# Kernel optimization log

Hardware: AMD Instinct MI355X
Metric: run time of the kernel (lower is better)

## Reference

```python
import jax, jax.numpy as jnp
import numpy as np

B, L, D, E, K, P = 1024, 320, 128, 8, 2, 96
NOISE_EPS = 0.01
LOSS_COEF = 0.01


def setup_inputs() -> dict:
    key = jax.random.key(0)
    ks = jax.random.split(key, 8)
    return {
        "x": jax.random.normal(ks[0], (B, L, D), jnp.float32),
        "x_mark_enc": jax.random.normal(ks[1], (B, L, 4), jnp.float32),
        "noise": jax.random.normal(ks[2], (B, E), jnp.float32),  # randn_like in torch
        "start_w": jax.random.normal(ks[3], (D, 1), jnp.float32) * 0.05,
        "start_b": jnp.zeros((1,), jnp.float32),
        "w_gate": jax.random.normal(ks[4], (L, E), jnp.float32) * 0.02,
        "w_noise": jax.random.normal(ks[5], (L, E), jnp.float32) * 0.02,
        "expert_w": jax.random.normal(ks[6], (E, L, P), jnp.float32) * (1.0 / np.sqrt(L)),
        "expert_b": jnp.zeros((E, P, D), jnp.float32),
    }


def _norm_cdf(v):
    return 0.5 * (1.0 + jax.lax.erf(v * (1.0 / np.sqrt(2.0)).astype(v.dtype) if hasattr((1.0 / np.sqrt(2.0)), 'astype') else v / jnp.sqrt(jnp.asarray(2.0, v.dtype))))


def _cdf(v):
    # standard normal CDF, Normal(0,1).cdf
    return 0.5 * (1.0 + jax.lax.erf(v / jnp.sqrt(jnp.asarray(2.0, v.dtype))))


def _cv_squared(v):
    eps = 1e-10
    return jnp.var(v, ddof=1) / (jnp.mean(v) ** 2 + eps)


def reference(x, x_mark_enc, noise, start_w, start_b, w_gate, w_noise, expert_b, expert_w):
    # --- noisy top-k gating (train mode) ---
    g = jnp.squeeze(x @ start_w, -1) + start_b  # [B, L]
    clean_logits = g @ w_gate                    # [B, E]
    noise_std = jax.nn.softplus(g @ w_noise) + NOISE_EPS
    noisy_logits = clean_logits + noise * noise_std

    top_logits, top_idx = jax.lax.top_k(noisy_logits, K + 1)  # [B, K+1]
    top_k_gates = jax.nn.softmax(top_logits[:, :K], axis=1)
    gates = jnp.zeros_like(noisy_logits).at[
        jnp.arange(noisy_logits.shape[0])[:, None], top_idx[:, :K]
    ].set(top_k_gates)  # [B, E] sparse gates (zeros elsewhere)

    # --- differentiable load via prob-in-top-k ---
    thr_in = top_logits[:, K:K + 1]       # (k+1)-th noisy value
    thr_out = top_logits[:, K - 1:K]      # k-th noisy value
    clean_c = jnp.where(jnp.isnan(clean_logits), 0.0, clean_logits)
    prob = jnp.where(
        noisy_logits > thr_in,
        _cdf((clean_c - thr_in) / noise_std),
        _cdf((clean_c - thr_out) / noise_std),
    )
    load = prob.sum(0)          # [E]
    importance = gates.sum(0)   # [E]
    balance_loss = LOSS_COEF * (_cv_squared(importance) + _cv_squared(load))

    # --- dispatch/combine: dense-equivalent of SparseDispatcher ---
    # expert e: out_e = einsum('bld,lp->bpd', x, W_e); combine weights = gates
    per_expert = jnp.einsum('bld,elp->ebpd', x, expert_w)          # [E, B, P, D]
    out = jnp.einsum('be,ebpd->bpd', gates, per_expert)
    out = out + jnp.einsum('be,epd->bpd', gates, expert_b)
    regu_sum = jnp.asarray(0.0, jnp.float32)
    return out, balance_loss, regu_sum
```

## Files before the change

kernel.cpp:

```cpp
#include <hip/hip_runtime.h>
#include <hip/hip_bf16.h>

#define Bn 1024
#define Lr 320
#define Dd 128
#define Ee 8
#define Pp 96

typedef short bf16x8 __attribute__((ext_vector_type(8)));
typedef float f32x4 __attribute__((ext_vector_type(4)));
typedef unsigned u32x4 __attribute__((ext_vector_type(4)));
typedef unsigned short u16;

__device__ __forceinline__ float cdf_f(float v) {
    return 0.5f * (1.0f + erff(v * 0.70710678118654752f));
}
__device__ __forceinline__ float softplus_f(float x) {
    return fmaxf(x, 0.0f) + log1pf(expf(-fabsf(x)));
}
__device__ __forceinline__ u16 f2bf(float f) {
    unsigned int u = __float_as_uint(f);
    return (u16)((u + 0x7fffu + ((u >> 16) & 1u)) >> 16);
}
__device__ __forceinline__ float bf2f(u16 u) {
    return __uint_as_float(((unsigned int)u) << 16);
}

__device__ __forceinline__ void gload16(const void* g, void* l) {
    __builtin_amdgcn_global_load_lds(
        (const __attribute__((address_space(1))) void*)g,
        (__attribute__((address_space(3))) void*)l, 16, 0, 0);
}

__global__ __launch_bounds__(256, 8) void g2_kernel(
    const float* __restrict__ x, const float* __restrict__ start_w,
    const float* __restrict__ start_b, const float* __restrict__ w_gate,
    const float* __restrict__ w_noise, float* __restrict__ zbuf)
{
    __shared__ float sred[16];
    const int t  = threadIdx.x;
    const int lc = blockIdx.x;
    const int b  = blockIdx.y;
    const float sb = start_b[0];
    const int f8 = t & 7;

    if (t < 16) sred[t] = 0.f;
    __syncthreads();

    float4 sw[4];
    #pragma unroll
    for (int j = 0; j < 4; ++j) sw[j] = ((const float4*)start_w)[f8 + 8 * j];

    const float* xb = x + ((size_t)b * Lr + lc * 64) * Dd;
    float zc = 0.f, zn = 0.f;
    #pragma unroll
    for (int p2 = 0; p2 < 2; ++p2) {
        const int r = p2 * 32 + (t >> 3);
        float acc = 0.f;
        #pragma unroll
        for (int j = 0; j < 4; ++j) {
            const float4 v = ((const float4*)(xb + (size_t)r * Dd))[f8 + 8 * j];
            acc += v.x * sw[j].x + v.y * sw[j].y + v.z * sw[j].z + v.w * sw[j].w;
        }
        #pragma unroll
        for (int off = 1; off <= 4; off <<= 1) acc += __shfl_xor(acc, off);
        const float gv = acc + sb;
        const int l = lc * 64 + r;
        zc += gv * w_gate[l * Ee + f8];
        zn += gv * w_noise[l * Ee + f8];
    }
    #pragma unroll
    for (int off = 8; off <= 32; off <<= 1) {
        zc += __shfl_xor(zc, off);
        zn += __shfl_xor(zn, off);
    }
    if ((t & 63) < 8) {
        atomicAdd(&sred[f8], zc);
        atomicAdd(&sred[8 + f8], zn);
    }
    __syncthreads();
    if (t < 16) zbuf[(b * 5 + lc) * 16 + t] = sred[t];
}

__global__ __launch_bounds__(256) void tk_tr_kernel(
    const float* __restrict__ zbuf, const float* __restrict__ noise,
    const float* __restrict__ ew, u16* __restrict__ wt,
    float* __restrict__ lossbuf, float* __restrict__ gates_out)
{
    __shared__ float tile[Pp * 33];
    const int t = threadIdx.x;

    if (blockIdx.x >= 4) {
        const int bx = blockIdx.x - 4;
        const int e  = bx / 10;
        const int l0 = (bx - 10 * e) * 32;
        #pragma unroll
        for (int i = 0; i < 12; ++i) {
            const int idx = t + 256 * i;
            const int lp = idx / 96, p = idx - 96 * lp;
            tile[p * 33 + lp] = ew[((size_t)e * Lr + l0 + lp) * Pp + p];
        }
        __syncthreads();
        #pragma unroll
        for (int i = 0; i < 6; ++i) {
            const int g = t + 256 * i;
            const int p = g >> 4, l2 = (g & 15) * 2;
            const unsigned pk = (unsigned)f2bf(tile[p * 33 + l2]) |
                                ((unsigned)f2bf(tile[p * 33 + l2 + 1]) << 16);
            *(unsigned*)&wt[((size_t)(e * Pp + p)) * Lr + l0 + l2] = pk;
        }
        return;
    }

    float* sred = tile;
    const int b = blockIdx.x * 256 + t;

    if (t < 16) sred[t] = 0.f;
    __syncthreads();

    float zc[8], zn[8], nsy[8], sdv[8];
    #pragma unroll
    for (int e = 0; e < 8; ++e) { zc[e] = 0.f; zn[e] = 0.f; }
    #pragma unroll
    for (int lc = 0; lc < 5; ++lc) {
        #pragma unroll
        for (int e = 0; e < 8; ++e) {
            zc[e] += zbuf[(b * 5 + lc) * 16 + e];
            zn[e] += zbuf[(b * 5 + lc) * 16 + 8 + e];
        }
    }
    #pragma unroll
    for (int e = 0; e < 8; ++e) {
        sdv[e] = softplus_f(zn[e]) + 0.01f;
        nsy[e] = zc[e] + noise[b * Ee + e] * sdv[e];
    }

    int i0 = -1, i1 = -1;
    float v0 = -INFINITY, v1 = -INFINITY, v2 = -INFINITY;
    #pragma unroll
    for (int i = 0; i < 8; ++i) if (nsy[i] > v0) { v0 = nsy[i]; i0 = i; }
    #pragma unroll
    for (int i = 0; i < 8; ++i) if (i != i0 && nsy[i] > v1) { v1 = nsy[i]; i1 = i; }
    #pragma unroll
    for (int i = 0; i < 8; ++i) if (i != i0 && i != i1 && nsy[i] > v2) { v2 = nsy[i]; }

    const float ex1 = expf(v1 - v0);
    const float den = 1.f + ex1;
    const float g0 = 1.f / den, g1 = ex1 / den;

    float im[8], pr[8];
    #pragma unroll
    for (int e = 0; e < 8; ++e) {
        im[e] = (e == i0) ? g0 : ((e == i1) ? g1 : 0.f);
        float c = zc[e];
        if (isnan(c)) c = 0.f;
        pr[e] = (nsy[e] > v2) ? cdf_f((c - v2) / sdv[e])
                              : cdf_f((c - v1) / sdv[e]);
        gates_out[b * Ee + e] = im[e];
    }

    #pragma unroll
    for (int off = 1; off <= 32; off <<= 1) {
        #pragma unroll
        for (int e = 0; e < 8; ++e) {
            pr[e] += __shfl_xor(pr[e], off);
            im[e] += __shfl_xor(im[e], off);
        }
    }
    if ((t & 63) == 0) {
        #pragma unroll
        for (int e = 0; e < 8; ++e) {
            atomicAdd(&sred[e], pr[e]);
            atomicAdd(&sred[8 + e], im[e]);
        }
    }
    __syncthreads();
    if (t < 16) lossbuf[blockIdx.x * 16 + t] = sred[t];
}

__global__ __launch_bounds__(512, 2) void mm_kernel(
    const float* __restrict__ x, const u16* __restrict__ wt,
    const float* __restrict__ expert_b, const float* __restrict__ gates,
    const float* __restrict__ lossbuf, float* __restrict__ out)
{
    __shared__ __align__(16) unsigned Ws[2][192 * 16];

    const int tid = threadIdx.x;

    if (blockIdx.x == 0 && tid == 0) {
        float lo[8], im[8];
        #pragma unroll
        for (int i = 0; i < 8; ++i) {
            lo[i] = lossbuf[i]      + lossbuf[16 + i] +
                    lossbuf[32 + i] + lossbuf[48 + i];
            im[i] = lossbuf[8 + i]  + lossbuf[24 + i] +
                    lossbuf[40 + i] + lossbuf[56 + i];
        }
        float ml = 0.f, mi = 0.f;
        #pragma unroll
        for (int i = 0; i < 8; ++i) { ml += lo[i]; mi += im[i]; }
        ml *= 0.125f; mi *= 0.125f;
        float sl = 0.f, si = 0.f;
        #pragma unroll
        for (int i = 0; i < 8; ++i) {
            const float dl = lo[i] - ml, di = im[i] - mi;
            sl += dl * dl; si += di * di;
        }
        const float cvl = (sl / 7.f) / (ml * ml + 1e-10f);
        const float cvi = (si / 7.f) / (mi * mi + 1e-10f);
        float* os = out + (size_t)Bn * Pp * Dd;
        os[0] = 0.01f * (cvi + cvl);
        os[1] = 0.0f;
    }

    const int b    = blockIdx.x;
    const int lane = tid & 63;
    const int wv   = tid >> 6;
    const int hh   = wv >> 2;
    const int nt   = wv & 3;
    const int quad = lane >> 4;
    const int r16  = lane & 15;

    int e0 = 0, e1 = 0; float g0 = 0.f, g1 = 0.f; int cnt = 0;
    #pragma unroll
    for (int e = 0; e < Ee; ++e) {
        const float gv = gates[b * Ee + e];
        if (gv != 0.f) {
            if (cnt == 0) { e0 = e; g0 = gv; }
            else if (cnt == 1) { e1 = e; g1 = gv; }
            ++cnt;
        }
    }

    const u16* w0r = wt + (size_t)e0 * Pp * Lr;
    const u16* w1r = wt + (size_t)e1 * Pp * Lr;

    const int d = hh * 64 + nt * 16 + r16;
    const float* xg = x + ((size_t)b * Lr + 8 * quad) * Dd + d;

    const int wrow = lane >> 2;
    const int wq   = lane & 3;

    auto STAGE_W = [&](int buf, int l0) {
        {
            const int c  = wv;
            const int r  = 16 * c + wrow;
            const int dw = (4 * wq) ^ ((r & 3) << 2);
            const u16* src = (c < 6) ? (w0r + (size_t)r * Lr)
                                     : (w1r + (size_t)(r - 96) * Lr);
            gload16(src + l0 + 2 * dw, (void*)&Ws[buf][c * 256]);
        }
        if (wv < 4) {
            const int c  = 8 + wv;
            const int r  = 16 * c + wrow;
            const int dw = (4 * wq) ^ ((r & 3) << 2);
            const u16* src = w1r + (size_t)(r - 96) * Lr;
            gload16(src + l0 + 2 * dw, (void*)&Ws[buf][c * 256]);
        }
    };

    float xa[8], xb8[8];
    auto LOADX = [&](float* dst, int l0) {
        #pragma unroll
        for (int k = 0; k < 8; ++k)
            dst[k] = xg[(size_t)(l0 + k) * Dd];
    };

    f32x4 a0[6], a1[6];
    #pragma unroll
    for (int m = 0; m < 6; ++m) {
        a0[m] = (f32x4){0.f, 0.f, 0.f, 0.f};
        a1[m] = (f32x4){0.f, 0.f, 0.f, 0.f};
    }

    const int wdw = (4 * quad) ^ ((r16 & 3) << 2);

    union UF { u32x4 q; bf16x8 v; unsigned u[4]; };

    auto COMPUTE = [&](int buf, const float* xv) {
        UF xf;
        #pragma unroll
        for (int k2 = 0; k2 < 4; ++k2)
            xf.u[k2] = (unsigned)f2bf(xv[2 * k2]) |
                       ((unsigned)f2bf(xv[2 * k2 + 1]) << 16);
        #pragma unroll
        for (int m = 0; m < 6; ++m) {
            UF f0, f1;
            f0.q = *(const u32x4*)&Ws[buf][(16 * m + r16) * 16 + wdw];
            f1.q = *(const u32x4*)&Ws[buf][(96 + 16 * m + r16) * 16 + wdw];
            a0[m] = __builtin_amdgcn_mfma_f32_16x16x32_bf16(f0.v, xf.v, a0[m], 0, 0, 0);
            a1[m] = __builtin_amdgcn_mfma_f32_16x16x32_bf16(f1.v, xf.v, a1[m], 0, 0, 0);
        }
    };

    STAGE_W(0, 0);
    LOADX(xa, 0);
    __syncthreads();

    #pragma unroll
    for (int t = 0; t < 10; t += 2) {
        STAGE_W(1, 32 * (t + 1));
        LOADX(xb8, 32 * (t + 1));
        COMPUTE(0, xa);
        __syncthreads();
        if (t + 2 < 10) {
            STAGE_W(0, 32 * (t + 2));
            LOADX(xa, 32 * (t + 2));
        }
        COMPUTE(1, xb8);
        __syncthreads();
    }

    const float* eb0 = expert_b + (size_t)e0 * Pp * Dd;
    const float* eb1 = expert_b + (size_t)e1 * Pp * Dd;
    #pragma unroll
    for (int m = 0; m < 6; ++m) {
        #pragma unroll
        for (int r = 0; r < 4; ++r) {
            const int p = 16 * m + 4 * quad + r;
            out[((size_t)b * Pp + p) * Dd + d] =
                g0 * (a0[m][r] + eb0[p * Dd + d]) +
                g1 * (a1[m][r] + eb1[p * Dd + d]);
        }
    }
}

extern "C" void kernel_launch(void* const* d_in, const int* in_sizes, int n_in,
                              void* d_out, int out_size, void* d_ws, size_t ws_size,
                              hipStream_t stream)
{
    const float* x        = (const float*)d_in[0];
    const float* noise    = (const float*)d_in[2];
    const float* start_w  = (const float*)d_in[3];
    const float* start_b  = (const float*)d_in[4];
    const float* w_gate   = (const float*)d_in[5];
    const float* w_noise  = (const float*)d_in[6];
    const float* expert_w = (const float*)d_in[7];
    const float* expert_b = (const float*)d_in[8];
    float* out            = (float*)d_out;

    float* gates   = (float*)d_ws;
    float* zbuf    = gates + Bn * Ee;
    float* lossbuf = zbuf + Bn * 80;
    u16*   wt      = (u16*)(lossbuf + 64);

    hipLaunchKernelGGL(g2_kernel, dim3(5, Bn), dim3(256), 0, stream,
                       x, start_w, start_b, w_gate, w_noise, zbuf);
    hipLaunchKernelGGL(tk_tr_kernel, dim3(84), dim3(256), 0, stream,
                       zbuf, noise, expert_w, wt, lossbuf, gates);
    hipLaunchKernelGGL(mm_kernel, dim3(Bn), dim3(512), 0, stream,
                       x, wt, expert_b, gates, lossbuf, out);
}
```

Before: 300.6 us.

## Fuse weight transpose into gating kernel and deepen x prefetch in matmul

Moves the expert-weight transpose/bf16 conversion into the gating-reduction kernel as extra blocks, so it overlaps with the x·start_w pass, and leaves a small top-k kernel on its own. In the main matmul kernel, x loads are issued one stage further ahead and barriers use partial vmcnt waits (keep 8 loads in flight) with sched_barrier, so global loads overlap MFMA work instead of being drained at every barrier. This adds hand-tuned waitcnt assumptions that could break if the compiler orders the loads differently.

```diff
diff --git a/kernel.cpp b/kernel.cpp
--- a/kernel.cpp
+++ b/kernel.cpp
@@ -32,68 +32,31 @@
         (__attribute__((address_space(3))) void*)l, 16, 0, 0);
 }
 
-__global__ __launch_bounds__(256, 8) void g2_kernel(
+__device__ __forceinline__ void bar_keep8() {
+    asm volatile("s_waitcnt vmcnt(8)" ::: "memory");
+    __builtin_amdgcn_s_barrier();
+    __builtin_amdgcn_sched_barrier(0);
+}
+__device__ __forceinline__ void bar_keep0() {
+    asm volatile("s_waitcnt vmcnt(0)" ::: "memory");
+    __builtin_amdgcn_s_barrier();
+    __builtin_amdgcn_sched_barrier(0);
+}
+
+__global__ __launch_bounds__(256, 8) void g2tr_kernel(
     const float* __restrict__ x, const float* __restrict__ start_w,
     const float* __restrict__ start_b, const float* __restrict__ w_gate,
-    const float* __restrict__ w_noise, float* __restrict__ zbuf)
-{
-    __shared__ float sred[16];
-    const int t  = threadIdx.x;
-    const int lc = blockIdx.x;
-    const int b  = blockIdx.y;
-    const float sb = start_b[0];
-    const int f8 = t & 7;
-
-    if (t < 16) sred[t] = 0.f;
-    __syncthreads();
-
-    float4 sw[4];
-    #pragma unroll
-    for (int j = 0; j < 4; ++j) sw[j] = ((const float4*)start_w)[f8 + 8 * j];
-
-    const float* xb = x + ((size_t)b * Lr + lc * 64) * Dd;
-    float zc = 0.f, zn = 0.f;
-    #pragma unroll
-    for (int p2 = 0; p2 < 2; ++p2) {
-        const int r = p2 * 32 + (t >> 3);
-        float acc = 0.f;
-        #pragma unroll
-        for (int j = 0; j < 4; ++j) {
-            const float4 v = ((const float4*)(xb + (size_t)r * Dd))[f8 + 8 * j];
-            acc += v.x * sw[j].x + v.y * sw[j].y + v.z * sw[j].z + v.w * sw[j].w;
-        }
-        #pragma unroll
-        for (int off = 1; off <= 4; off <<= 1) acc += __shfl_xor(acc, off);
-        const float gv = acc + sb;
-        const int l = lc * 64 + r;
-        zc += gv * w_gate[l * Ee + f8];
-        zn += gv * w_noise[l * Ee + f8];
-    }
-    #pragma unroll
-    for (int off = 8; off <= 32; off <<= 1) {
-        zc += __shfl_xor(zc, off);
-        zn += __shfl_xor(zn, off);
-    }
-    if ((t & 63) < 8) {
-        atomicAdd(&sred[f8], zc);
-        atomicAdd(&sred[8 + f8], zn);
-    }
-    __syncthreads();
-    if (t < 16) zbuf[(b * 5 + lc) * 16 + t] = sred[t];
-}
-
-__global__ __launch_bounds__(256) void tk_tr_kernel(
-    const float* __restrict__ zbuf, const float* __restrict__ noise,
-    const float* __restrict__ ew, u16* __restrict__ wt,
-    float* __restrict__ lossbuf, float* __restrict__ gates_out)
+    const float* __restrict__ w_noise, const float* __restrict__ ew,
+    u16* __restrict__ wt, float* __restrict__ zbuf)
 {
     __shared__ float tile[Pp * 33];
+    __shared__ float sred[16];
     const int t = threadIdx.x;
 
-    if (blockIdx.x >= 4) {
-        const int bx = blockIdx.x - 4;
-        const int e  = bx / 10;
-        const int l0 = (bx - 10 * e) * 32;
+    if (blockIdx.y < 16) {
+        const int chunk = blockIdx.y * 5 + blockIdx.x;
+        const int e  = chunk / 10;
+        const int l0 = (chunk - 10 * e) * 32;
         #pragma unroll
         for (int i = 0; i < 12; ++i) {
             const int idx = t + 256 * i;
@@ -112,7 +75,55 @@
         return;
     }
 
-    float* sred = tile;
+    const int lc = blockIdx.x;
+    const int b  = blockIdx.y - 16;
+    const float sb = start_b[0];
+    const int f8 = t & 7;
+
+    if (t < 16) sred[t] = 0.f;
+    __syncthreads();
+
+    float4 sw[4];
+    #pragma unroll
+    for (int j = 0; j < 4; ++j) sw[j] = ((const float4*)start_w)[f8 + 8 * j];
+
+    const float* xb = x + ((size_t)b * Lr + lc * 64) * Dd;
+    float zc = 0.f, zn = 0.f;
+    #pragma unroll
+    for (int p2 = 0; p2 < 2; ++p2) {
+        const int r = p2 * 32 + (t >> 3);
+        float acc = 0.f;
+        #pragma unroll
+        for (int j = 0; j < 4; ++j) {
+            const float4 v = ((const float4*)(xb + (size_t)r * Dd))[f8 + 8 * j];
+            acc += v.x * sw[j].x + v.y * sw[j].y + v.z * sw[j].z + v.w * sw[j].w;
+        }
+        #pragma unroll
+        for (int off = 1; off <= 4; off <<= 1) acc += __shfl_xor(acc, off);
+        const float gv = acc + sb;
+        const int l = lc * 64 + r;
+        zc += gv * w_gate[l * Ee + f8];
+        zn += gv * w_noise[l * Ee + f8];
+    }
+    #pragma unroll
+    for (int off = 8; off <= 32; off <<= 1) {
+        zc += __shfl_xor(zc, off);
+        zn += __shfl_xor(zn, off);
+    }
+    if ((t & 63) < 8) {
+        atomicAdd(&sred[f8], zc);
+        atomicAdd(&sred[8 + f8], zn);
+    }
+    __syncthreads();
+    if (t < 16) zbuf[(b * 5 + lc) * 16 + t] = sred[t];
+}
+
+__global__ __launch_bounds__(256) void topk_kernel(
+    const float* __restrict__ zbuf, const float* __restrict__ noise,
+    float* __restrict__ lossbuf, float* __restrict__ gates_out)
+{
+    __shared__ float sred[16];
+    const int t = threadIdx.x;
     const int b = blockIdx.x * 256 + t;
 
     if (t < 16) sred[t] = 0.f;
@@ -277,12 +288,13 @@
 
     union UF { u32x4 q; bf16x8 v; unsigned u[4]; };
 
-    auto COMPUTE = [&](int buf, const float* xv) {
-        UF xf;
+    auto PACK = [&](UF& xf, const float* xv) {
         #pragma unroll
         for (int k2 = 0; k2 < 4; ++k2)
             xf.u[k2] = (unsigned)f2bf(xv[2 * k2]) |
                        ((unsigned)f2bf(xv[2 * k2 + 1]) << 16);
+    };
+    auto MFMA12 = [&](int buf, const UF& xf) {
         #pragma unroll
         for (int m = 0; m < 6; ++m) {
             UF f0, f1;
@@ -295,20 +307,29 @@
 
     STAGE_W(0, 0);
     LOADX(xa, 0);
-    __syncthreads();
+    LOADX(xb8, 32);
+    bar_keep8();
 
     #pragma unroll
     for (int t = 0; t < 10; t += 2) {
         STAGE_W(1, 32 * (t + 1));
-        LOADX(xb8, 32 * (t + 1));
-        COMPUTE(0, xa);
-        __syncthreads();
+        {
+            UF xf;
+            PACK(xf, xa);
+            if (t + 2 < 10) LOADX(xa, 32 * (t + 2));
+            MFMA12(0, xf);
+        }
+        if (t + 2 < 10) bar_keep8(); else bar_keep0();
+        if (t + 2 < 10) STAGE_W(0, 32 * (t + 2));
+        {
+            UF xf;
+            PACK(xf, xb8);
+            if (t + 3 < 10) LOADX(xb8, 32 * (t + 3));
+            MFMA12(1, xf);
+        }
         if (t + 2 < 10) {
-            STAGE_W(0, 32 * (t + 2));
-            LOADX(xa, 32 * (t + 2));
-        }
-        COMPUTE(1, xb8);
-        __syncthreads();
+            if (t + 3 < 10) bar_keep8(); else bar_keep0();
+        }
     }
 
     const float* eb0 = expert_b + (size_t)e0 * Pp * Dd;
@@ -344,10 +365,11 @@
     float* lossbuf = zbuf + Bn * 80;
     u16*   wt      = (u16*)(lossbuf + 64);
 
-    hipLaunchKernelGGL(g2_kernel, dim3(5, Bn), dim3(256), 0, stream,
-                       x, start_w, start_b, w_gate, w_noise, zbuf);
-    hipLaunchKernelGGL(tk_tr_kernel, dim3(84), dim3(256), 0, stream,
-                       zbuf, noise, expert_w, wt, lossbuf, gates);
+    hipLaunchKernelGGL(g2tr_kernel, dim3(5, 1040), dim3(256), 0, stream,
+                       x, start_w, start_b, w_gate, w_noise,
+                       expert_w, wt, zbuf);
+    hipLaunchKernelGGL(topk_kernel, dim3(Bn / 256), dim3(256), 0, stream,
+                       zbuf, noise, lossbuf, gates);
     hipLaunchKernelGGL(mm_kernel, dim3(Bn), dim3(512), 0, stream,
                        x, wt, expert_b, gates, lossbuf, out);
 }
```

After: 302.3 us. No clear change (+0.6%).
